# Kernel optimization log

Hardware: AMD Instinct MI355X
Metric: run time of the kernel (lower is better)

Reference implementation:

```python
import jax, jax.numpy as jnp
import numpy as np

N_EMBD = 2048
N_HEAD = 16
D_HEAD = N_EMBD // N_HEAD


def setup_inputs() -> dict:
    key = jax.random.key(0)
    k1, k2, k3 = jax.random.split(key, 3)
    x = jax.random.normal(k1, (2, 2048, N_EMBD), dtype=jnp.float32)
    # torch Linear stores weight as [out, in]; kept in that layout
    w_qkv = jax.random.normal(k2, (3 * N_EMBD, N_EMBD), dtype=jnp.float32) * (1.0 / np.sqrt(N_EMBD))
    w_out = jax.random.normal(k3, (N_EMBD, N_EMBD), dtype=jnp.float32) * (1.0 / np.sqrt(N_EMBD))
    return {"x": x, "w_qkv": w_qkv, "w_out": w_out}


def reference(x, w_qkv, w_out):
    B, T, C = x.shape
    H, D = N_HEAD, D_HEAD
    qkv = jnp.einsum('btc,oc->bto', x, w_qkv)            # [B,T,3C]
    qkv = qkv.reshape(B, T, 3, H, D)
    q = jnp.transpose(qkv[:, :, 0], (0, 2, 1, 3))        # [B,H,T,D]
    k = jnp.transpose(qkv[:, :, 1], (0, 2, 1, 3))
    v = jnp.transpose(qkv[:, :, 2], (0, 2, 1, 3))
    scale = 1.0 / np.sqrt(D).astype(np.float32)
    att = jnp.einsum('bhqd,bhkd->bhqk', q, k) * scale    # [B,H,T,T]
    causal = jnp.tril(jnp.ones((T, T), dtype=bool))
    att = jnp.where(causal[None, None], att, jnp.finfo(att.dtype).min)
    att = jax.nn.softmax(att, axis=-1)
    y = jnp.einsum('bhqk,bhkd->bhqd', att, v)            # [B,H,T,D]
    y = jnp.transpose(y, (0, 2, 1, 3)).reshape(B, T, C)
    return jnp.einsum('btc,oc->bto', y, w_out)
```

## Files before the change

kernel.cpp:

```cpp
#include <hip/hip_runtime.h>
#include <stdint.h>


typedef __attribute__((ext_vector_type(8))) short bf16x8;
typedef __attribute__((ext_vector_type(8))) unsigned short u16x8;
typedef __attribute__((ext_vector_type(4))) unsigned short u16x4;
typedef __attribute__((ext_vector_type(4))) float f32x4;

#define MFMA16(a, b, c) __builtin_amdgcn_mfma_f32_16x16x32_bf16((a), (b), (c), 0, 0, 0)

__device__ __forceinline__ unsigned short f2bf(float f) {
  union { float f; uint32_t u; } v; v.f = f;
  uint32_t r = v.u + 0x7FFFu + ((v.u >> 16) & 1u);
  return (unsigned short)(r >> 16);
}

__device__ __forceinline__ void gld_lds16(const unsigned short* g, unsigned short* lds) {
  __builtin_amdgcn_global_load_lds(
      (const __attribute__((address_space(1))) void*)g,
      (__attribute__((address_space(3))) void*)lds, 16, 0, 0);
}

__global__ __launch_bounds__(256) void cvt_bf16(const float* __restrict__ in,
                                                unsigned short* __restrict__ out, int n8) {
  int stride = gridDim.x * blockDim.x;
  for (int i = blockIdx.x * blockDim.x + threadIdx.x; i < n8; i += stride) {
    float4 a = reinterpret_cast<const float4*>(in)[i * 2];
    float4 b = reinterpret_cast<const float4*>(in)[i * 2 + 1];
    u16x8 o;
    o[0] = f2bf(a.x); o[1] = f2bf(a.y); o[2] = f2bf(a.z); o[3] = f2bf(a.w);
    o[4] = f2bf(b.x); o[5] = f2bf(b.y); o[6] = f2bf(b.z); o[7] = f2bf(b.w);
    reinterpret_cast<u16x8*>(out)[i] = o;
  }
}

__device__ __forceinline__ void gemm128_core(const unsigned short* __restrict__ A,
                                             const unsigned short* __restrict__ Bt,
                                             int K, int brow, int bcol,
                                             unsigned short* lds_a, unsigned short* lds_b,
                                             f32x4 acc[4][4]) {
  const int tid = threadIdx.x;
  const int l   = tid & 63;
  const int w   = tid >> 6;
  const int wr  = (w >> 1) << 6;
  const int wc  = (w & 1) << 6;

  const int srow = tid >> 2;
  const int sswz = (tid & 3) ^ ((srow >> 1) & 3);
  const unsigned short* gA0 = A  + (size_t)(brow + srow) * K + 8 * sswz;
  const unsigned short* gA1 = gA0 + (size_t)64 * K;
  const unsigned short* gB0 = Bt + (size_t)(bcol + srow) * K + 8 * sswz;
  const unsigned short* gB1 = gB0 + (size_t)64 * K;

  unsigned short* la0 = lds_a + tid * 8;
  unsigned short* la1 = lds_a + (256 + tid) * 8;
  unsigned short* lb0 = lds_b + tid * 8;
  unsigned short* lb1 = lds_b + (256 + tid) * 8;

  const int fm    = l & 15;
  const int fswz8 = 8 * ((l >> 4) ^ ((fm >> 1) & 3));

  for (int k0 = 0; k0 < K; k0 += 32) {
    gld_lds16(gA0, la0);
    gld_lds16(gA1, la1);
    gld_lds16(gB0, lb0);
    gld_lds16(gB1, lb1);
    gA0 += 32; gA1 += 32; gB0 += 32; gB1 += 32;
    __syncthreads();
    bf16x8 af[4], bfv[4];
#pragma unroll
    for (int i = 0; i < 4; i++)
      af[i] = *(const bf16x8*)&lds_a[(wr + i * 16 + fm) * 32 + fswz8];
#pragma unroll
    for (int j = 0; j < 4; j++)
      bfv[j] = *(const bf16x8*)&lds_b[(wc + j * 16 + fm) * 32 + fswz8];
#pragma unroll
    for (int i = 0; i < 4; i++)
#pragma unroll
      for (int j = 0; j < 4; j++)
        acc[i][j] = MFMA16(af[i], bfv[j], acc[i][j]);
    __syncthreads();
  }
}

__global__ __launch_bounds__(256) void gemm_qkv(const unsigned short* __restrict__ xb,
                                                const unsigned short* __restrict__ wqb,
                                                unsigned short* __restrict__ Qb,
                                                unsigned short* __restrict__ Kb,
                                                unsigned short* __restrict__ Vtb) {
  __shared__ alignas(16) unsigned short lds_a[128 * 32];
  __shared__ alignas(16) unsigned short lds_b[128 * 32];
  f32x4 acc[4][4];
#pragma unroll
  for (int i = 0; i < 4; i++)
#pragma unroll
    for (int j = 0; j < 4; j++) acc[i][j] = (f32x4){0.f, 0.f, 0.f, 0.f};

  const int brow = blockIdx.y << 7;
  const int bcol = blockIdx.x << 7;
  gemm128_core(xb, wqb, 2048, brow, bcol, lds_a, lds_b, acc);

  const int l = threadIdx.x & 63;
  const int w = threadIdx.x >> 6;
  const int wr = (w >> 1) << 6, wc = (w & 1) << 6;
  const int which = bcol >> 11;
  const int bh = ((brow >> 11) << 4) | ((bcol >> 7) & 15);
  const int tbase = (brow & 2047) + wr + ((l >> 4) << 2);

#pragma unroll
  for (int i = 0; i < 4; i++) {
    const int t0 = tbase + i * 16;
#pragma unroll
    for (int j = 0; j < 4; j++) {
      const int d = wc + j * 16 + (l & 15);
      if (which == 2) {
        u16x4 pk;
#pragma unroll
        for (int r = 0; r < 4; r++) pk[r] = f2bf(acc[i][j][r]);
        *reinterpret_cast<u16x4*>(&Vtb[((size_t)bh * 128 + d) * 2048 + t0]) = pk;
      } else {
        unsigned short* dst = (which == 0 ? Qb : Kb) + ((size_t)bh * 2048 + t0) * 128 + d;
#pragma unroll
        for (int r = 0; r < 4; r++) dst[(size_t)r * 128] = f2bf(acc[i][j][r]);
      }
    }
  }
}

__global__ __launch_bounds__(256) void gemm_out(const unsigned short* __restrict__ yb,
                                                const unsigned short* __restrict__ wob,
                                                float* __restrict__ out) {
  __shared__ alignas(16) unsigned short lds_a[128 * 32];
  __shared__ alignas(16) unsigned short lds_b[128 * 32];
  f32x4 acc[4][4];
#pragma unroll
  for (int i = 0; i < 4; i++)
#pragma unroll
    for (int j = 0; j < 4; j++) acc[i][j] = (f32x4){0.f, 0.f, 0.f, 0.f};

  const int brow = blockIdx.y << 7;
  const int bcol = blockIdx.x << 7;
  gemm128_core(yb, wob, 2048, brow, bcol, lds_a, lds_b, acc);

  const int l = threadIdx.x & 63;
  const int w = threadIdx.x >> 6;
  const int wr = (w >> 1) << 6, wc = (w & 1) << 6;
#pragma unroll
  for (int i = 0; i < 4; i++) {
    const int m0 = brow + wr + i * 16 + ((l >> 4) << 2);
#pragma unroll
    for (int j = 0; j < 4; j++) {
      const int n = bcol + wc + j * 16 + (l & 15);
#pragma unroll
      for (int r = 0; r < 4; r++) out[(size_t)(m0 + r) * 2048 + n] = acc[i][j][r];
    }
  }
}

__device__ __forceinline__ void stage_kv64(const unsigned short* __restrict__ Kg,
                                           const unsigned short* __restrict__ Vg,
                                           int kv0, unsigned short* dk,
                                           unsigned short* dv, int tid) {
#pragma unroll
  for (int c = 0; c < 4; c++) {
    int s = c * 256 + tid;
    int row = s >> 4, g = s & 15;
    gld_lds16(&Kg[(size_t)(kv0 + row) * 128 + 8 * (g ^ (row & 7))], &dk[s * 8]);
  }
#pragma unroll
  for (int c = 0; c < 4; c++) {
    int s = c * 256 + tid;
    int row = s >> 3, g = s & 7;
    gld_lds16(&Vg[(size_t)row * 2048 + kv0 + 8 * (g ^ (row & 7))], &dv[s * 8]);
  }
}

__global__ __launch_bounds__(256) void attn_kernel(const unsigned short* __restrict__ Qb,
                                                   const unsigned short* __restrict__ Kb,
                                                   const unsigned short* __restrict__ Vtb,
                                                   unsigned short* __restrict__ Yb) {
  __shared__ alignas(16) unsigned short lds_k[2][64 * 128];
  __shared__ alignas(16) unsigned short lds_v[2][128 * 64];
  __shared__ alignas(16) unsigned short p_lds[4][16 * 64];

  const int tid = threadIdx.x;
  const int l = tid & 63;
  const int w = tid >> 6;

  const int bid = blockIdx.x;
  const int xcd = bid & 7;
  const int loc = bid >> 3;
  const int bh = xcd * 4 + (loc >> 4);
  const int jidx = loc & 15;

  const int b = bh >> 4, h = bh & 15;
  const float SC = 0.12752585f;

  const unsigned short* Qg = Qb + (size_t)bh * 2048 * 128;
  const unsigned short* Kg = Kb + (size_t)bh * 2048 * 128;
  const unsigned short* Vg = Vtb + (size_t)bh * 128 * 2048;

  for (int ph = 0; ph < 2; ph++) {
    const int h64 = (ph == 0) ? jidx : (31 - jidx);
    const int q0 = h64 << 6;
    const int qw0 = q0 + (w << 4);

    bf16x8 qf[4];
#pragma unroll
    for (int ds = 0; ds < 4; ds++)
      qf[ds] = *(const bf16x8*)&Qg[(size_t)(qw0 + (l & 15)) * 128 + ds * 32 + 8 * (l >> 4)];

    f32x4 yacc[8];
#pragma unroll
    for (int dt = 0; dt < 8; dt++) yacc[dt] = (f32x4){0.f, 0.f, 0.f, 0.f};
    float mrow[4], lrow[4];
#pragma unroll
    for (int r = 0; r < 4; r++) { mrow[r] = -1e30f; lrow[r] = 0.f; }

    const int nkv = h64 + 1;

    stage_kv64(Kg, Vg, 0, lds_k[0], lds_v[0], tid);
    asm volatile("s_waitcnt vmcnt(0)" ::: "memory");
    __syncthreads();

    for (int t = 0; t < nkv; t++) {
      const int kv0 = t << 6;
      const int buf = t & 1;
      const unsigned short* kb = lds_k[buf];
      const unsigned short* vb = lds_v[buf];
      if (t + 1 < nkv)
        stage_kv64(Kg, Vg, kv0 + 64, lds_k[buf ^ 1], lds_v[buf ^ 1], tid);

      if (kv0 <= qw0 + 15) {
        f32x4 sfr[4];
#pragma unroll
        for (int kt = 0; kt < 4; kt++) {
          const int kr = kt * 16 + (l & 15);
          f32x4 s4 = (f32x4){0.f, 0.f, 0.f, 0.f};
#pragma unroll
          for (int ds = 0; ds < 4; ds++) {
            bf16x8 kfr = *(const bf16x8*)&kb[kr * 128 + 8 * (((ds << 2) + (l >> 4)) ^ (kr & 7))];
            s4 = MFMA16(qf[ds], kfr, s4);
          }
          sfr[kt] = s4;
        }
        const bool need_mask = (kv0 + 63 > qw0);
#pragma unroll
        for (int kt = 0; kt < 4; kt++)
#pragma unroll
          for (int r = 0; r < 4; r++) {
            float sv = sfr[kt][r] * SC;
            if (need_mask) {
              int qa = qw0 + ((l >> 4) << 2) + r;
              int ka = kv0 + kt * 16 + (l & 15);
              sv = (ka > qa) ? -1e30f : sv;
            }
            sfr[kt][r] = sv;
          }
        float rmax[4];
#pragma unroll
        for (int r = 0; r < 4; r++) {
          float m = fmaxf(fmaxf(sfr[0][r], sfr[1][r]), fmaxf(sfr[2][r], sfr[3][r]));
          m = fmaxf(m, __shfl_xor(m, 1));
          m = fmaxf(m, __shfl_xor(m, 2));
          m = fmaxf(m, __shfl_xor(m, 4));
          m = fmaxf(m, __shfl_xor(m, 8));
          rmax[r] = m;
        }
        bool sm = (rmax[0] <= mrow[0] + 8.f) && (rmax[1] <= mrow[1] + 8.f) &&
                  (rmax[2] <= mrow[2] + 8.f) && (rmax[3] <= mrow[3] + 8.f);
        if (!__all(sm)) {
          float f[4];
#pragma unroll
          for (int r = 0; r < 4; r++) {
            float mn = fmaxf(mrow[r], rmax[r]);
            f[r] = exp2f(mrow[r] - mn);
            mrow[r] = mn;
            lrow[r] *= f[r];
          }
#pragma unroll
          for (int dt = 0; dt < 8; dt++)
#pragma unroll
            for (int r = 0; r < 4; r++) yacc[dt][r] *= f[r];
        }
        float rsum[4] = {0.f, 0.f, 0.f, 0.f};
#pragma unroll
        for (int kt = 0; kt < 4; kt++)
#pragma unroll
          for (int r = 0; r < 4; r++) {
            float p = exp2f(sfr[kt][r] - mrow[r]);
            rsum[r] += p;
            int row = ((l >> 4) << 2) + r;
            int k = kt * 16 + (l & 15);
            p_lds[w][row * 64 + (((k >> 3) ^ (row & 7)) << 3) + (k & 7)] = f2bf(p);
          }
#pragma unroll
        for (int r = 0; r < 4; r++) {
          float s = rsum[r];
          s += __shfl_xor(s, 1);
          s += __shfl_xor(s, 2);
          s += __shfl_xor(s, 4);
          s += __shfl_xor(s, 8);
          lrow[r] += s;
        }

        asm volatile("s_waitcnt lgkmcnt(0)" ::: "memory");
        __builtin_amdgcn_sched_barrier(0);

#pragma unroll
        for (int ks = 0; ks < 2; ks++) {
          const int prow = l & 15;
          bf16x8 pa = *(const bf16x8*)&p_lds[w][prow * 64 + ((((ks << 2) + (l >> 4)) ^ (prow & 7)) << 3)];
#pragma unroll
          for (int dt = 0; dt < 8; dt++) {
            const int d = dt * 16 + (l & 15);
            bf16x8 vv = *(const bf16x8*)&vb[d * 64 + ((((ks << 2) + (l >> 4)) ^ (d & 7)) << 3)];
            yacc[dt] = MFMA16(pa, vv, yacc[dt]);
          }
        }
      }
      asm volatile("s_waitcnt vmcnt(0)" ::: "memory");
      __syncthreads();
    }
#pragma unroll
    for (int dt = 0; dt < 8; dt++)
#pragma unroll
      for (int r = 0; r < 4; r++) {
        int qa = qw0 + ((l >> 4) << 2) + r;
        Yb[((size_t)(b * 2048 + qa)) * 2048 + h * 128 + dt * 16 + (l & 15)] =
            f2bf(yacc[dt][r] / lrow[r]);
      }
  }
}

extern "C" void kernel_launch(void* const* d_in, const int* in_sizes, int n_in,
                              void* d_out, int out_size, void* d_ws, size_t ws_size,
                              hipStream_t stream) {
  const float* x    = (const float*)d_in[0];
  const float* wqkv = (const float*)d_in[1];
  const float* wout = (const float*)d_in[2];
  float* out = (float*)d_out;

  unsigned short* ws  = (unsigned short*)d_ws;
  unsigned short* xb  = ws;
  unsigned short* wqb = xb + (size_t)8388608;
  unsigned short* wob = wqb + (size_t)12582912;
  unsigned short* Qb  = wob + (size_t)4194304;
  unsigned short* Kb  = Qb + (size_t)8388608;
  unsigned short* Vtb = Kb + (size_t)8388608;
  unsigned short* Yb  = Vtb + (size_t)8388608;

  cvt_bf16<<<1024, 256, 0, stream>>>(x, xb, 8388608 / 8);
  cvt_bf16<<<1024, 256, 0, stream>>>(wqkv, wqb, 12582912 / 8);
  cvt_bf16<<<512, 256, 0, stream>>>(wout, wob, 4194304 / 8);
  gemm_qkv<<<dim3(48, 32), 256, 0, stream>>>(xb, wqb, Qb, Kb, Vtb);
  attn_kernel<<<512, 256, 0, stream>>>(Qb, Kb, Vtb, Yb);
  gemm_out<<<dim3(16, 32), 256, 0, stream>>>(Yb, wob, out);
}
```

Before: 286.1 us.

## Process paired causal query tiles together sharing each staged KV tile

```diff
diff --git a/kernel.cpp b/kernel.cpp
--- a/kernel.cpp
+++ b/kernel.cpp
@@ -175,10 +175,108 @@
   }
 }
 
-__global__ __launch_bounds__(256) void attn_kernel(const unsigned short* __restrict__ Qb,
-                                                   const unsigned short* __restrict__ Kb,
-                                                   const unsigned short* __restrict__ Vtb,
-                                                   unsigned short* __restrict__ Yb) {
+__device__ __forceinline__ void attn_tile_step(const bf16x8 qf[4], f32x4 yacc[8],
+                                               float mrow[4], float lrow[4],
+                                               int qw0, int kv0,
+                                               const unsigned short* kb,
+                                               const unsigned short* vb,
+                                               unsigned short* pw, int l) {
+  const float SC = 0.12752585f;
+  f32x4 sfr[4];
+  __builtin_amdgcn_s_setprio(1);
+#pragma unroll
+  for (int kt = 0; kt < 4; kt++) {
+    const int kr = kt * 16 + (l & 15);
+    f32x4 s4 = (f32x4){0.f, 0.f, 0.f, 0.f};
+#pragma unroll
+    for (int ds = 0; ds < 4; ds++) {
+      bf16x8 kfr = *(const bf16x8*)&kb[kr * 128 + 8 * (((ds << 2) + (l >> 4)) ^ (kr & 7))];
+      s4 = MFMA16(qf[ds], kfr, s4);
+    }
+    sfr[kt] = s4;
+  }
+  __builtin_amdgcn_s_setprio(0);
+  const bool need_mask = (kv0 + 63 > qw0);
+#pragma unroll
+  for (int kt = 0; kt < 4; kt++)
+#pragma unroll
+    for (int r = 0; r < 4; r++) {
+      float sv = sfr[kt][r] * SC;
+      if (need_mask) {
+        int qa = qw0 + ((l >> 4) << 2) + r;
+        int ka = kv0 + kt * 16 + (l & 15);
+        sv = (ka > qa) ? -1e30f : sv;
+      }
+      sfr[kt][r] = sv;
+    }
+  float rmax[4];
+#pragma unroll
+  for (int r = 0; r < 4; r++) {
+    float m = fmaxf(fmaxf(sfr[0][r], sfr[1][r]), fmaxf(sfr[2][r], sfr[3][r]));
+    m = fmaxf(m, __shfl_xor(m, 1));
+    m = fmaxf(m, __shfl_xor(m, 2));
+    m = fmaxf(m, __shfl_xor(m, 4));
+    m = fmaxf(m, __shfl_xor(m, 8));
+    rmax[r] = m;
+  }
+  bool sm = (rmax[0] <= mrow[0] + 8.f) && (rmax[1] <= mrow[1] + 8.f) &&
+            (rmax[2] <= mrow[2] + 8.f) && (rmax[3] <= mrow[3] + 8.f);
+  if (!__all(sm)) {
+    float f[4];
+#pragma unroll
+    for (int r = 0; r < 4; r++) {
+      float mn = fmaxf(mrow[r], rmax[r]);
+      f[r] = exp2f(mrow[r] - mn);
+      mrow[r] = mn;
+      lrow[r] *= f[r];
+    }
+#pragma unroll
+    for (int dt = 0; dt < 8; dt++)
+#pragma unroll
+      for (int r = 0; r < 4; r++) yacc[dt][r] *= f[r];
+  }
+  float rsum[4] = {0.f, 0.f, 0.f, 0.f};
+#pragma unroll
+  for (int kt = 0; kt < 4; kt++)
+#pragma unroll
+    for (int r = 0; r < 4; r++) {
+      float p = exp2f(sfr[kt][r] - mrow[r]);
+      rsum[r] += p;
+      int row = ((l >> 4) << 2) + r;
+      int k = kt * 16 + (l & 15);
+      pw[row * 64 + (((k >> 3) ^ (row & 7)) << 3) + (k & 7)] = f2bf(p);
+    }
+#pragma unroll
+  for (int r = 0; r < 4; r++) {
+    float s = rsum[r];
+    s += __shfl_xor(s, 1);
+    s += __shfl_xor(s, 2);
+    s += __shfl_xor(s, 4);
+    s += __shfl_xor(s, 8);
+    lrow[r] += s;
+  }
+  asm volatile("s_waitcnt lgkmcnt(0)" ::: "memory");
+  __builtin_amdgcn_sched_barrier(0);
+  __builtin_amdgcn_s_setprio(1);
+#pragma unroll
+  for (int ks = 0; ks < 2; ks++) {
+    const int prow = l & 15;
+    bf16x8 pa = *(const bf16x8*)&pw[prow * 64 + ((((ks << 2) + (l >> 4)) ^ (prow & 7)) << 3)];
+#pragma unroll
+    for (int dt = 0; dt < 8; dt++) {
+      const int d = dt * 16 + (l & 15);
+      bf16x8 vv = *(const bf16x8*)&vb[d * 64 + ((((ks << 2) + (l >> 4)) ^ (d & 7)) << 3)];
+      yacc[dt] = MFMA16(pa, vv, yacc[dt]);
+    }
+  }
+  __builtin_amdgcn_s_setprio(0);
+  asm volatile("s_waitcnt lgkmcnt(0)" ::: "memory");
+}
+
+__global__ __launch_bounds__(256, 2) void attn_kernel(const unsigned short* __restrict__ Qb,
+                                                      const unsigned short* __restrict__ Kb,
+                                                      const unsigned short* __restrict__ Vtb,
+                                                      unsigned short* __restrict__ Yb) {
   __shared__ alignas(16) unsigned short lds_k[2][64 * 128];
   __shared__ alignas(16) unsigned short lds_v[2][128 * 64];
   __shared__ alignas(16) unsigned short p_lds[4][16 * 64];
@@ -194,143 +292,68 @@
   const int jidx = loc & 15;
 
   const int b = bh >> 4, h = bh & 15;
-  const float SC = 0.12752585f;
 
   const unsigned short* Qg = Qb + (size_t)bh * 2048 * 128;
   const unsigned short* Kg = Kb + (size_t)bh * 2048 * 128;
   const unsigned short* Vg = Vtb + (size_t)bh * 128 * 2048;
 
-  for (int ph = 0; ph < 2; ph++) {
-    const int h64 = (ph == 0) ? jidx : (31 - jidx);
-    const int q0 = h64 << 6;
-    const int qw0 = q0 + (w << 4);
-
-    bf16x8 qf[4];
-#pragma unroll
-    for (int ds = 0; ds < 4; ds++)
-      qf[ds] = *(const bf16x8*)&Qg[(size_t)(qw0 + (l & 15)) * 128 + ds * 32 + 8 * (l >> 4)];
-
-    f32x4 yacc[8];
-#pragma unroll
-    for (int dt = 0; dt < 8; dt++) yacc[dt] = (f32x4){0.f, 0.f, 0.f, 0.f};
-    float mrow[4], lrow[4];
-#pragma unroll
-    for (int r = 0; r < 4; r++) { mrow[r] = -1e30f; lrow[r] = 0.f; }
-
-    const int nkv = h64 + 1;
-
-    stage_kv64(Kg, Vg, 0, lds_k[0], lds_v[0], tid);
+  const int j_lo = jidx, j_hi = 31 - jidx;
+  const int qw0_lo = (j_lo << 6) + (w << 4);
+  const int qw0_hi = (j_hi << 6) + (w << 4);
+
+  bf16x8 qf_lo[4], qf_hi[4];
+#pragma unroll
+  for (int ds = 0; ds < 4; ds++) {
+    qf_lo[ds] = *(const bf16x8*)&Qg[(size_t)(qw0_lo + (l & 15)) * 128 + ds * 32 + 8 * (l >> 4)];
+    qf_hi[ds] = *(const bf16x8*)&Qg[(size_t)(qw0_hi + (l & 15)) * 128 + ds * 32 + 8 * (l >> 4)];
+  }
+
+  f32x4 yacc_lo[8], yacc_hi[8];
+#pragma unroll
+  for (int dt = 0; dt < 8; dt++) {
+    yacc_lo[dt] = (f32x4){0.f, 0.f, 0.f, 0.f};
+    yacc_hi[dt] = (f32x4){0.f, 0.f, 0.f, 0.f};
+  }
+  float mrow_lo[4], lrow_lo[4], mrow_hi[4], lrow_hi[4];
+#pragma unroll
+  for (int r = 0; r < 4; r++) {
+    mrow_lo[r] = -1e30f; lrow_lo[r] = 0.f;
+    mrow_hi[r] = -1e30f; lrow_hi[r] = 0.f;
+  }
+
+  const int nkv = j_hi + 1;
+
+  stage_kv64(Kg, Vg, 0, lds_k[0], lds_v[0], tid);
+  asm volatile("s_waitcnt vmcnt(0)" ::: "memory");
+  __syncthreads();
+
+  for (int t = 0; t < nkv; t++) {
+    const int kv0 = t << 6;
+    const int buf = t & 1;
+    const unsigned short* kb = lds_k[buf];
+    const unsigned short* vb = lds_v[buf];
+    if (t + 1 < nkv)
+      stage_kv64(Kg, Vg, kv0 + 64, lds_k[buf ^ 1], lds_v[buf ^ 1], tid);
+
+    if (kv0 <= qw0_lo + 15)
+      attn_tile_step(qf_lo, yacc_lo, mrow_lo, lrow_lo, qw0_lo, kv0, kb, vb, p_lds[w], l);
+    attn_tile_step(qf_hi, yacc_hi, mrow_hi, lrow_hi, qw0_hi, kv0, kb, vb, p_lds[w], l);
+
     asm volatile("s_waitcnt vmcnt(0)" ::: "memory");
     __syncthreads();
-
-    for (int t = 0; t < nkv; t++) {
-      const int kv0 = t << 6;
-      const int buf = t & 1;
-      const unsigned short* kb = lds_k[buf];
-      const unsigned short* vb = lds_v[buf];
-      if (t + 1 < nkv)
-        stage_kv64(Kg, Vg, kv0 + 64, lds_k[buf ^ 1], lds_v[buf ^ 1], tid);
-
-      if (kv0 <= qw0 + 15) {
-        f32x4 sfr[4];
-#pragma unroll
-        for (int kt = 0; kt < 4; kt++) {
-          const int kr = kt * 16 + (l & 15);
-          f32x4 s4 = (f32x4){0.f, 0.f, 0.f, 0.f};
-#pragma unroll
-          for (int ds = 0; ds < 4; ds++) {
-            bf16x8 kfr = *(const bf16x8*)&kb[kr * 128 + 8 * (((ds << 2) + (l >> 4)) ^ (kr & 7))];
-            s4 = MFMA16(qf[ds], kfr, s4);
-          }
-          sfr[kt] = s4;
-        }
-        const bool need_mask = (kv0 + 63 > qw0);
-#pragma unroll
-        for (int kt = 0; kt < 4; kt++)
-#pragma unroll
-          for (int r = 0; r < 4; r++) {
-            float sv = sfr[kt][r] * SC;
-            if (need_mask) {
-              int qa = qw0 + ((l >> 4) << 2) + r;
-              int ka = kv0 + kt * 16 + (l & 15);
-              sv = (ka > qa) ? -1e30f : sv;
-            }
-            sfr[kt][r] = sv;
-          }
-        float rmax[4];
-#pragma unroll
-        for (int r = 0; r < 4; r++) {
-          float m = fmaxf(fmaxf(sfr[0][r], sfr[1][r]), fmaxf(sfr[2][r], sfr[3][r]));
-          m = fmaxf(m, __shfl_xor(m, 1));
-          m = fmaxf(m, __shfl_xor(m, 2));
-          m = fmaxf(m, __shfl_xor(m, 4));
-          m = fmaxf(m, __shfl_xor(m, 8));
-          rmax[r] = m;
-        }
-        bool sm = (rmax[0] <= mrow[0] + 8.f) && (rmax[1] <= mrow[1] + 8.f) &&
-                  (rmax[2] <= mrow[2] + 8.f) && (rmax[3] <= mrow[3] + 8.f);
-        if (!__all(sm)) {
-          float f[4];
-#pragma unroll
-          for (int r = 0; r < 4; r++) {
-            float mn = fmaxf(mrow[r], rmax[r]);
-            f[r] = exp2f(mrow[r] - mn);
-            mrow[r] = mn;
-            lrow[r] *= f[r];
-          }
-#pragma unroll
-          for (int dt = 0; dt < 8; dt++)
-#pragma unroll
-            for (int r = 0; r < 4; r++) yacc[dt][r] *= f[r];
-        }
-        float rsum[4] = {0.f, 0.f, 0.f, 0.f};
-#pragma unroll
-        for (int kt = 0; kt < 4; kt++)
-#pragma unroll
-          for (int r = 0; r < 4; r++) {
-            float p = exp2f(sfr[kt][r] - mrow[r]);
-            rsum[r] += p;
-            int row = ((l >> 4) << 2) + r;
-            int k = kt * 16 + (l & 15);
-            p_lds[w][row * 64 + (((k >> 3) ^ (row & 7)) << 3) + (k & 7)] = f2bf(p);
-          }
-#pragma unroll
-        for (int r = 0; r < 4; r++) {
-          float s = rsum[r];
-          s += __shfl_xor(s, 1);
-          s += __shfl_xor(s, 2);
-          s += __shfl_xor(s, 4);
-          s += __shfl_xor(s, 8);
-          lrow[r] += s;
-        }
-
-        asm volatile("s_waitcnt lgkmcnt(0)" ::: "memory");
-        __builtin_amdgcn_sched_barrier(0);
-
-#pragma unroll
-        for (int ks = 0; ks < 2; ks++) {
-          const int prow = l & 15;
-          bf16x8 pa = *(const bf16x8*)&p_lds[w][prow * 64 + ((((ks << 2) + (l >> 4)) ^ (prow & 7)) << 3)];
-#pragma unroll
-          for (int dt = 0; dt < 8; dt++) {
-            const int d = dt * 16 + (l & 15);
-            bf16x8 vv = *(const bf16x8*)&vb[d * 64 + ((((ks << 2) + (l >> 4)) ^ (d & 7)) << 3)];
-            yacc[dt] = MFMA16(pa, vv, yacc[dt]);
-          }
-        }
-      }
-      asm volatile("s_waitcnt vmcnt(0)" ::: "memory");
-      __syncthreads();
-    }
-#pragma unroll
-    for (int dt = 0; dt < 8; dt++)
-#pragma unroll
-      for (int r = 0; r < 4; r++) {
-        int qa = qw0 + ((l >> 4) << 2) + r;
-        Yb[((size_t)(b * 2048 + qa)) * 2048 + h * 128 + dt * 16 + (l & 15)] =
-            f2bf(yacc[dt][r] / lrow[r]);
-      }
-  }
+  }
+
+#pragma unroll
+  for (int dt = 0; dt < 8; dt++)
+#pragma unroll
+    for (int r = 0; r < 4; r++) {
+      int qa_lo = qw0_lo + ((l >> 4) << 2) + r;
+      int qa_hi = qw0_hi + ((l >> 4) << 2) + r;
+      Yb[((size_t)(b * 2048 + qa_lo)) * 2048 + h * 128 + dt * 16 + (l & 15)] =
+          f2bf(yacc_lo[dt][r] / lrow_lo[r]);
+      Yb[((size_t)(b * 2048 + qa_hi)) * 2048 + h * 128 + dt * 16 + (l & 15)] =
+          f2bf(yacc_hi[dt][r] / lrow_hi[r]);
+    }
 }
 
 extern "C" void kernel_launch(void* const* d_in, const int* in_sizes, int n_in,
```

Measured after the change: 284.3 us. No clear change (-0.6%).
